# Kernel tuning notes

Hardware: AMD Instinct MI355X
Metric: run time of the kernel (lower is better)

## Reference

```python
import jax, jax.numpy as jnp
import numpy as np

D_MODEL = 1024
NUM_HEADS = 16
D_K = D_MODEL // NUM_HEADS  # 64
MAX_REL_POS = 16
B, SQ, SK = 1, 2048, 2048


def setup_inputs() -> dict:
    key = jax.random.key(0)
    ks = jax.random.split(key, 12)
    s = 0.02
    inp = {
        "query": jax.random.normal(ks[0], (B, SQ, D_MODEL), jnp.float32),
        "key": jax.random.normal(ks[1], (B, SK, D_MODEL), jnp.float32),
        "value": jax.random.normal(ks[2], (B, SK, D_MODEL), jnp.float32),
        "mask": jnp.ones((B, 1, SQ, SK), dtype=bool),
        # torch nn.Linear weights: y = x @ W.T + b
        "Wq": jax.random.normal(ks[3], (D_MODEL, D_MODEL), jnp.float32) * s,
        "bq": jnp.zeros((D_MODEL,), jnp.float32),
        "Wk": jax.random.normal(ks[4], (D_MODEL, D_MODEL), jnp.float32) * s,
        "bk": jnp.zeros((D_MODEL,), jnp.float32),
        "Wv": jax.random.normal(ks[5], (D_MODEL, D_MODEL), jnp.float32) * s,
        "bv": jnp.zeros((D_MODEL,), jnp.float32),
        "Wo": jax.random.normal(ks[6], (D_MODEL, D_MODEL), jnp.float32) * s,
        "bo": jnp.zeros((D_MODEL,), jnp.float32),
        # RelativePosition embedding table: [2*P+1, d_k]
        "rel_table": jax.random.normal(ks[7], (2 * MAX_REL_POS + 1, D_K), jnp.float32) * s,
    }
    return inp


def reference(query, key, value, mask, Wq, bq, Wk, bk, Wv, bv, Wo, bo, rel_table):
    b, sq, d = query.shape
    sk = key.shape[1]
    H, dk = NUM_HEADS, D_K

    Q = (query @ Wq.T + bq).reshape(b, sq, H, dk).transpose(0, 2, 1, 3)  # [B,H,Sq,dk]
    K = (key @ Wk.T + bk).reshape(b, sk, H, dk).transpose(0, 2, 1, 3)    # [B,H,Sk,dk]
    V = (value @ Wv.T + bv).reshape(b, sk, H, dk).transpose(0, 2, 1, 3)  # [B,H,Sk,dk]

    scores = jnp.einsum("bhqd,bhkd->bhqk", Q, K)  # [B,H,Sq,Sk]

    # relative-position bias on keys: ref_pos[i,j] = clip(j-i, -P, P) + P
    pos = jnp.clip(jnp.arange(sk)[None, :] - jnp.arange(sq)[:, None],
                   -MAX_REL_POS, MAX_REL_POS) + MAX_REL_POS  # [Sq,Sk] int
    rel = rel_table[pos]  # [Sq,Sk,dk]
    scores = scores + jnp.einsum("bhqd,qkd->bhqk", Q, rel)

    scores = scores / jnp.sqrt(jnp.float32(dk))
    scores = jnp.where(mask, scores, jnp.float32(-1e12))
    attn = jax.nn.softmax(scores, axis=-1)

    x = jnp.einsum("bhqk,bhkd->bhqd", attn, V)  # [B,H,Sq,dk]
    x = x.transpose(0, 2, 1, 3).reshape(b, sq, d)
    return x @ Wo.T + bo
```

## Files before the change

### kernel.cpp

```cpp
#include <hip/hip_runtime.h>

#define S_LEN 2048
#define DM    1024
#define NH    16
#define DK    64
#define NP    33
#define QB    128
#define KB    64
#define NSPLIT 3

#define LOG2E 1.44269504088896340736f

typedef __attribute__((ext_vector_type(8))) __bf16 bf16x8;
typedef __attribute__((ext_vector_type(4))) float f32x4;
typedef __attribute__((ext_vector_type(16))) float f32x16;
typedef __attribute__((ext_vector_type(8))) unsigned short u16x8;

__device__ __forceinline__ unsigned short f2bf(float f) {
  unsigned int x = __float_as_uint(f);
  x += 0x7fffu + ((x >> 16) & 1u);
  return (unsigned short)(x >> 16);
}
__device__ __forceinline__ float bf2f(unsigned short u) {
  return __uint_as_float(((unsigned int)u) << 16);
}
__device__ __forceinline__ f32x4 mfma16(bf16x8 a, bf16x8 b, f32x4 c) {
  return __builtin_amdgcn_mfma_f32_16x16x32_bf16(a, b, c, 0, 0, 0);
}
__device__ __forceinline__ f32x16 mfma32(bf16x8 a, bf16x8 b, f32x16 c) {
  return __builtin_amdgcn_mfma_f32_32x32x16_bf16(a, b, c, 0, 0, 0);
}
__device__ __forceinline__ unsigned cvtpk(float lo, float hi) {
  unsigned r;
  asm("v_cvt_pk_bf16_f32 %0, %1, %2" : "=v"(r) : "v"(lo), "v"(hi));
  return r;
}
__device__ __forceinline__ void halfswap(unsigned &a, unsigned &b) {
  asm volatile("v_permlane32_swap_b32 %0, %1" : "+v"(a), "+v"(b));
}
__device__ __forceinline__ void gload16(const void* g, void* l) {
  __builtin_amdgcn_global_load_lds(
      (const __attribute__((address_space(1))) unsigned int*)g,
      (__attribute__((address_space(3))) unsigned int*)l, 16, 0, 0);
}
#define WAITCNT(n) asm volatile("s_waitcnt vmcnt(" #n ")" ::: "memory")
#define LGKM0 asm volatile("s_waitcnt lgkmcnt(0)" ::: "memory")
__device__ __forceinline__ void bar() { __builtin_amdgcn_s_barrier(); }
__device__ __forceinline__ u16x8 pk8(float4 a, float4 b) {
  union { unsigned u[4]; u16x8 v; } f;
  f.u[0] = cvtpk(a.x, a.y); f.u[1] = cvtpk(a.z, a.w);
  f.u[2] = cvtpk(b.x, b.y); f.u[3] = cvtpk(b.z, b.w);
  return f.v;
}

__global__ __launch_bounds__(256) void cvt_w_kernel(
    const float* wq, const float* wk, const float* wv, const float* wo,
    unsigned short* wqo, unsigned short* wko, unsigned short* wvo, unsigned short* woo)
{
#pragma unroll
  for (int j = 0; j < 4; j++) {
    int idx = blockIdx.x * 1024 + j * 256 + threadIdx.x;
    int sel = idx >> 17, off = idx & 131071;
    const float* s = sel == 0 ? wq : (sel == 1 ? wk : (sel == 2 ? wv : wo));
    unsigned short* d = sel == 0 ? wqo : (sel == 1 ? wko : (sel == 2 ? wvo : woo));
    const float* p = s + (size_t)off * 8;
    u16x8 o;
#pragma unroll
    for (int e = 0; e < 8; e++) o[e] = f2bf(p[e]);
    *(u16x8*)(d + (size_t)off * 8) = o;
  }
}

__global__ __launch_bounds__(256, 3) void gemm_qkv_kernel(
    const float* X0, const float* X1, const float* X2,
    const unsigned short* W0, const unsigned short* W1, const unsigned short* W2,
    const float* b0, const float* b1, const float* b2,
    unsigned short* O0, unsigned short* O1, unsigned short* VTout)
{
  __shared__ unsigned short As[2][64 * 64];
  __shared__ unsigned short Bs[2][128 * 64];
  int bid = blockIdx.x;
  int xcd = bid & 7, local = bid >> 3;
  int z = local >> 5, r = local & 31;
  int bn = (r & 7) * 128;
  int bm = (xcd * 4 + (r >> 3)) * 64;

  const float* A          = z == 0 ? X0 : (z == 1 ? X1 : X2);
  const unsigned short* W = z == 0 ? W0 : (z == 1 ? W1 : W2);
  const float* bias       = z == 0 ? b0 : (z == 1 ? b1 : b2);
  float scale             = z == 0 ? 0.125f * LOG2E : 1.f;

  int tid = threadIdx.x, lane = tid & 63, w = tid >> 6;
  int r15 = lane & 15, g = lane >> 4;
  int wm = (w & 1) * 32, wn = (w >> 1) * 64;
  f32x4 acc[2][4];
#pragma unroll
  for (int mi = 0; mi < 2; mi++)
#pragma unroll
    for (int ni = 0; ni < 4; ni++)
#pragma unroll
      for (int i = 0; i < 4; i++) acc[mi][ni][i] = 0.f;

  int ra0 = tid >> 3, sa0 = ((tid & 7) ^ (ra0 & 7)) * 8;
  int ra1 = ra0 + 32, sa1 = (((tid + 256) & 7) ^ (ra1 & 7)) * 8;
  const float* aF0 = &A[(size_t)(bm + ra0) * DM + sa0];
  const float* aF1 = &A[(size_t)(bm + ra1) * DM + sa1];
  const unsigned short* bSrc[4];
#pragma unroll
  for (int j = 0; j < 4; j++) {
    int cb = j * 256 + tid;
    int rb = cb >> 3, sb = ((cb & 7) ^ (rb & 7)) * 8;
    bSrc[j] = &W[(size_t)(bn + rb) * DM + sb];
  }

  float4 a00, a01, a10, a11;
  auto LOAD_A = [&](int k0) {
    a00 = *(const float4*)(aF0 + k0);     a01 = *(const float4*)(aF0 + k0 + 4);
    a10 = *(const float4*)(aF1 + k0);     a11 = *(const float4*)(aF1 + k0 + 4);
  };
  auto STAGE_B = [&](int b, int k0) {
#pragma unroll
    for (int j = 0; j < 4; j++) gload16(bSrc[j] + k0, &Bs[b][(j * 256 + tid) * 8]);
  };
  auto WRITE_A = [&](int b) {
    *(u16x8*)&As[b][tid * 8]         = pk8(a00, a01);
    *(u16x8*)&As[b][(tid + 256) * 8] = pk8(a10, a11);
  };

  const int NS = DM / 64;
  STAGE_B(0, 0);
  LOAD_A(0);
  WAITCNT(0);
  WRITE_A(0);
  LGKM0;
  bar();

  for (int s = 0; s < NS; s++) {
    int cur = s & 1;
    int k0 = s * 64;
    if (s + 1 < NS) { STAGE_B(cur ^ 1, k0 + 64); LOAD_A(k0 + 64); }
    bf16x8 af[2][2], bfr[4][2];
#pragma unroll
    for (int mi = 0; mi < 2; mi++) {
      int row = wm + mi * 16 + r15;
#pragma unroll
      for (int hf = 0; hf < 2; hf++)
        af[mi][hf] = *(const bf16x8*)&As[cur][row * 64 + (((hf * 4 + g) ^ (row & 7)) << 3)];
    }
#pragma unroll
    for (int ni = 0; ni < 4; ni++) {
      int row = wn + ni * 16 + r15;
#pragma unroll
      for (int hf = 0; hf < 2; hf++)
        bfr[ni][hf] = *(const bf16x8*)&Bs[cur][row * 64 + (((hf * 4 + g) ^ (row & 7)) << 3)];
    }
    __builtin_amdgcn_s_setprio(1);
#pragma unroll
    for (int hf = 0; hf < 2; hf++)
#pragma unroll
      for (int mi = 0; mi < 2; mi++)
#pragma unroll
        for (int ni = 0; ni < 4; ni++)
          acc[mi][ni] = mfma16(af[mi][hf], bfr[ni][hf], acc[mi][ni]);
    __builtin_amdgcn_s_setprio(0);
    if (s + 1 < NS) {
      WAITCNT(0);
      WRITE_A(cur ^ 1);
    }
    LGKM0;
    bar();
  }

  if (z < 2) {
    unsigned short* O = z == 0 ? O0 : O1;
#pragma unroll
    for (int mi = 0; mi < 2; mi++)
#pragma unroll
      for (int ni = 0; ni < 4; ni++) {
        int col = bn + wn + ni * 16 + r15;
        float bv = bias[col];
#pragma unroll
        for (int i = 0; i < 4; i++) {
          int row = bm + wm + mi * 16 + g * 4 + i;
          O[(size_t)row * DM + col] = f2bf((acc[mi][ni][i] + bv) * scale);
        }
      }
  } else {
    unsigned short* Tl = (unsigned short*)Bs;
    const int TP = 72;
#pragma unroll
    for (int mi = 0; mi < 2; mi++)
#pragma unroll
      for (int ni = 0; ni < 4; ni++) {
        int colL = wn + ni * 16 + r15;
        float bv = bias[bn + colL];
#pragma unroll
        for (int i = 0; i < 4; i++) {
          int rowL = wm + mi * 16 + g * 4 + i;
          Tl[colL * TP + rowL] = f2bf(acc[mi][ni][i] + bv);
        }
      }
    __syncthreads();
#pragma unroll
    for (int i = 0; i < 4; i++) {
      int c = i * 256 + tid;
      int colL = c >> 3, k8 = (c & 7) * 8;
      u16x8 vv = *(const u16x8*)&Tl[colL * TP + k8];
      *(u16x8*)&VTout[(size_t)(bn + colL) * S_LEN + bm + k8] = vv;
    }
  }
}

template<int MR, int NR, int F32OUT>
__device__ __forceinline__ void gemm_body(
    const unsigned short* __restrict__ A, const unsigned short* __restrict__ W,
    const float* __restrict__ bias, unsigned short* __restrict__ outb,
    float* __restrict__ outf, int N, int K, int bm, int bn, float scale)
{
  __shared__ unsigned short As[2][MR * 32 * 64];
  __shared__ unsigned short Bs[2][NR * 32 * 64];
  int tid = threadIdx.x, lane = tid & 63, w = tid >> 6;
  int r15 = lane & 15, g = lane >> 4;
  int wm = (w & 1) * (MR * 16), wn = (w >> 1) * (NR * 16);
  f32x4 acc[MR][NR];
#pragma unroll
  for (int mi = 0; mi < MR; mi++)
#pragma unroll
    for (int ni = 0; ni < NR; ni++)
#pragma unroll
      for (int i = 0; i < 4; i++) acc[mi][ni][i] = 0.f;

  int lc = w * 64 + lane;
  int lrow = lc >> 3;
  int lk = ((lc & 7) ^ (lrow & 7)) * 8;
  const unsigned short* aS = &A[(size_t)(bm + lrow) * K + lk];
  const unsigned short* bS = &W[(size_t)(bn + lrow) * K + lk];
  int wOff = w * 512;

  auto STAGE = [&](int b, int k0) {
#pragma unroll
    for (int j = 0; j < MR; j++)
      gload16(aS + (size_t)(32 * j) * K + k0, &As[b][j * 2048 + wOff]);
#pragma unroll
    for (int j = 0; j < NR; j++)
      gload16(bS + (size_t)(32 * j) * K + k0, &Bs[b][j * 2048 + wOff]);
  };

  const int NS = K / 64;
  STAGE(0, 0);
  WAITCNT(0);
  bar();
  for (int s = 0; s < NS; s++) {
    int cur = s & 1;
    int k0 = s * 64;
    if (s + 1 < NS) STAGE(cur ^ 1, k0 + 64);
    bf16x8 af[MR][2], bfr[NR][2];
#pragma unroll
    for (int mi = 0; mi < MR; mi++) {
      int row = wm + mi * 16 + r15;
#pragma unroll
      for (int hf = 0; hf < 2; hf++)
        af[mi][hf] = *(const bf16x8*)&As[cur][row * 64 + (((hf * 4 + g) ^ (row & 7)) << 3)];
    }
#pragma unroll
    for (int ni = 0; ni < NR; ni++) {
      int row = wn + ni * 16 + r15;
#pragma unroll
      for (int hf = 0; hf < 2; hf++)
        bfr[ni][hf] = *(const bf16x8*)&Bs[cur][row * 64 + (((hf * 4 + g) ^ (row & 7)) << 3)];
    }
    __builtin_amdgcn_s_setprio(1);
#pragma unroll
    for (int hf = 0; hf < 2; hf++)
#pragma unroll
      for (int mi = 0; mi < MR; mi++)
#pragma unroll
        for (int ni = 0; ni < NR; ni++)
          acc[mi][ni] = mfma16(af[mi][hf], bfr[ni][hf], acc[mi][ni]);
    __builtin_amdgcn_s_setprio(0);
    WAITCNT(0);
    bar();
  }
#pragma unroll
  for (int mi = 0; mi < MR; mi++)
#pragma unroll
    for (int ni = 0; ni < NR; ni++) {
      int col = bn + wn + ni * 16 + r15;
      float bv = bias[col];
#pragma unroll
      for (int i = 0; i < 4; i++) {
        int row = bm + wm + mi * 16 + g * 4 + i;
        float v = (acc[mi][ni][i] + bv) * scale;
        if (F32OUT) outf[(size_t)row * N + col] = v;
        else        outb[(size_t)row * N + col] = f2bf(v);
      }
    }
}

__global__ __launch_bounds__(256, 2) void gemm_out_kernel(
    const unsigned short* A, const unsigned short* W, const float* bias, float* out)
{
  int bid = blockIdx.x;
  int xcd = bid & 7, local = bid >> 3;
  int bn = (local & 15) * 64;
  int bm = (xcd * 4 + (local >> 4)) * 64;
  gemm_body<2, 2, 1>(A, W, bias, nullptr, out, DM, DM, bm, bn, 1.f);
}

__global__ __launch_bounds__(256) void qrel_kernel(
    const unsigned short* __restrict__ Qb, const float* __restrict__ rel,
    unsigned short* __restrict__ QRbT)
{
  __shared__ float rels[NP * DK];
  int h = blockIdx.y;
  int tid = threadIdx.x;
  int q = blockIdx.x * 256 + tid;
  for (int i = tid; i < NP * DK; i += 256) rels[i] = rel[i];
  __syncthreads();
  float qv[DK];
  const unsigned short* qp = &Qb[(size_t)q * DM + h * DK];
#pragma unroll
  for (int j = 0; j < 8; j++) {
    u16x8 v = *(const u16x8*)&qp[j * 8];
#pragma unroll
    for (int e = 0; e < 8; e++) qv[j * 8 + e] = bf2f(v[e]);
  }
  int qt = q >> 7, qloc = q & 127;
  unsigned short* outp = &QRbT[((size_t)(h * 16 + qt) * NP) * QB + qloc];
  for (int p = 0; p < NP; p++) {
    float s = 0.f;
#pragma unroll
    for (int d = 0; d < DK; d++) s += qv[d] * rels[p * DK + d];
    outp[p * QB] = f2bf(s);
  }
}

__global__ __launch_bounds__(256, 3) void attn_kernel(
    const unsigned short* __restrict__ Qb, const unsigned short* __restrict__ Kb,
    const unsigned short* __restrict__ VT, const unsigned short* __restrict__ QRbT,
    unsigned short* __restrict__ Opart, float* __restrict__ ml)
{
  __shared__ unsigned short Ks[2][KB * DK];
  __shared__ unsigned short Vs[2][DK * KB];
  __shared__ unsigned short QRs[NP * QB];

  int bid = blockIdx.x;
  int wid = (bid & 7) * 96 + (bid >> 3);
  int h  = wid / 48;
  int rem = wid - h * 48;
  int split = rem >> 4;
  int qt = rem & 15;
  int q0 = qt * QB;
  int tstart = split * 11;
  int ts = split == 2 ? 10 : 11;

  int tid = threadIdx.x;
  int l = tid & 63, w = tid >> 6;
  int lq = l & 31, hi = l >> 5;

  int c0 = tid, c1 = tid + 256;
  int r0 = c0 >> 3, s0 = ((c0 & 7) ^ (r0 & 7)) * 8;
  int r1 = c1 >> 3, s1 = ((c1 & 7) ^ (r1 & 7)) * 8;
  int db0 = w * 512, db1 = 2048 + w * 512;
  const unsigned short* Ksrc0 = &Kb[(size_t)r0 * DM + h * DK + s0];
  const unsigned short* Ksrc1 = &Kb[(size_t)r1 * DM + h * DK + s1];
  const unsigned short* Vsrc0 = &VT[((size_t)h * DK + r0) * S_LEN + s0];
  const unsigned short* Vsrc1 = &VT[((size_t)h * DK + r1) * S_LEN + s1];

  auto STAGE = [&](int buf, int kb) {
    gload16(Ksrc0 + (size_t)kb * DM, &Ks[buf][db0]);
    gload16(Ksrc1 + (size_t)kb * DM, &Ks[buf][db1]);
    gload16(Vsrc0 + kb, &Vs[buf][db0]);
    gload16(Vsrc1 + kb, &Vs[buf][db1]);
  };

  int kb0 = tstart * KB;
  STAGE(0, kb0);

  {
    const u16x8* qsrc = (const u16x8*)&QRbT[(size_t)(h * 16 + qt) * NP * QB];
    u16x8* qdst = (u16x8*)QRs;
    for (int i = tid; i < NP * QB / 8; i += 256) qdst[i] = qsrc[i];
  }

  int qglob = q0 + w * 32 + lq;
  int qcol = w * 32 + lq;
  const unsigned short* qp = &Qb[(size_t)qglob * DM + h * DK + hi * 8];
  bf16x8 qfs[4];
#pragma unroll
  for (int s = 0; s < 4; s++) qfs[s] = *(const bf16x8*)&qp[s * 16];

  float m_i = -1e30f, l_i = 0.f;
  f32x16 o0, o1;
#pragma unroll
  for (int r = 0; r < 16; r++) { o0[r] = 0.f; o1[r] = 0.f; }

  asm volatile("s_waitcnt vmcnt(0) lgkmcnt(0)" ::: "memory");
  bar();

  for (int t = 0; t < ts; t++) {
    int buf = t & 1;
    int kbase = (tstart + t) * KB;
    if (t + 1 < ts) STAGE(buf ^ 1, kbase + KB);

    f32x16 sT0, sT1;
#pragma unroll
    for (int r = 0; r < 16; r++) { sT0[r] = 0.f; sT1[r] = 0.f; }
    __builtin_amdgcn_s_setprio(1);
#pragma unroll
    for (int s = 0; s < 4; s++) {
      int ch = s * 2 + hi;
      bf16x8 k0 = *(const bf16x8*)&Ks[buf][(lq) * DK + ((ch ^ (lq & 7)) << 3)];
      bf16x8 k1 = *(const bf16x8*)&Ks[buf][(32 + lq) * DK + ((ch ^ (lq & 7)) << 3)];
      sT0 = mfma32(k0, qfs[s], sT0);
      sT1 = mfma32(k1, qfs[s], sT1);
    }
    __builtin_amdgcn_s_setprio(0);

    bool hiC = (kbase - (q0 + QB - 1)) >= 16;
    bool loC = ((kbase + KB - 1) - q0) <= -16;
    float c_u = 0.f;
    if (hiC || loC) {
      c_u = bf2f(QRs[(hiC ? 32 : 0) * QB + qcol]);
    } else {
#pragma unroll
      for (int r = 0; r < 16; r++) {
        int km = (r & 3) + ((r >> 2) << 3) + (hi << 2);
        int d0 = kbase + km - qglob;
        int i0 = d0 < -16 ? 0 : (d0 > 16 ? 32 : d0 + 16);
        sT0[r] += bf2f(QRs[i0 * QB + qcol]);
        int d1 = d0 + 32;
        int i1 = d1 < -16 ? 0 : (d1 > 16 ? 32 : d1 + 16);
        sT1[r] += bf2f(QRs[i1 * QB + qcol]);
      }
    }

    float a0 = fmaxf(sT0[0], sT1[0]), a1 = fmaxf(sT0[1], sT1[1]);
    float a2 = fmaxf(sT0[2], sT1[2]), a3 = fmaxf(sT0[3], sT1[3]);
#pragma unroll
    for (int r = 4; r < 16; r += 4) {
      a0 = fmaxf(a0, fmaxf(sT0[r], sT1[r]));
      a1 = fmaxf(a1, fmaxf(sT0[r + 1], sT1[r + 1]));
      a2 = fmaxf(a2, fmaxf(sT0[r + 2], sT1[r + 2]));
      a3 = fmaxf(a3, fmaxf(sT0[r + 3], sT1[r + 3]));
    }
    float tm = fmaxf(fmaxf(a0, a1), fmaxf(a2, a3));
    tm = fmaxf(tm, __shfl_xor(tm, 32));
    float eff = tm + c_u;
    if (!__all(eff <= m_i + 11.5f)) {
      float mn = fmaxf(m_i, eff);
      float sc = __builtin_amdgcn_exp2f(m_i - mn);
      m_i = mn; l_i *= sc;
#pragma unroll
      for (int r = 0; r < 16; r++) { o0[r] *= sc; o1[r] *= sc; }
    }
    float mc = m_i - c_u;
    float p[32];
    float ls0 = 0.f, ls1 = 0.f, ls2 = 0.f, ls3 = 0.f;
#pragma unroll
    for (int r = 0; r < 16; r += 4) {
      p[r]     = __builtin_amdgcn_exp2f(sT0[r] - mc);     ls0 += p[r];
      p[r + 1] = __builtin_amdgcn_exp2f(sT0[r + 1] - mc); ls1 += p[r + 1];
      p[r + 2] = __builtin_amdgcn_exp2f(sT0[r + 2] - mc); ls2 += p[r + 2];
      p[r + 3] = __builtin_amdgcn_exp2f(sT0[r + 3] - mc); ls3 += p[r + 3];
    }
#pragma unroll
    for (int r = 0; r < 16; r += 4) {
      p[16 + r]     = __builtin_amdgcn_exp2f(sT1[r] - mc);     ls0 += p[16 + r];
      p[16 + r + 1] = __builtin_amdgcn_exp2f(sT1[r + 1] - mc); ls1 += p[16 + r + 1];
      p[16 + r + 2] = __builtin_amdgcn_exp2f(sT1[r + 2] - mc); ls2 += p[16 + r + 2];
      p[16 + r + 3] = __builtin_amdgcn_exp2f(sT1[r + 3] - mc); ls3 += p[16 + r + 3];
    }
    float ls = (ls0 + ls1) + (ls2 + ls3);
    ls += __shfl_xor(ls, 32);
    l_i += ls;

    bf16x8 pf[4];
#pragma unroll
    for (int kg = 0; kg < 2; kg++) {
      const float* pp = &p[kg * 16];
#pragma unroll
      for (int s2 = 0; s2 < 2; s2++) {
        unsigned b1 = cvtpk(pp[s2 * 8 + 0], pp[s2 * 8 + 1]);
        unsigned b2 = cvtpk(pp[s2 * 8 + 4], pp[s2 * 8 + 5]);
        unsigned b3 = cvtpk(pp[s2 * 8 + 2], pp[s2 * 8 + 3]);
        unsigned b4 = cvtpk(pp[s2 * 8 + 6], pp[s2 * 8 + 7]);
        halfswap(b1, b2); halfswap(b3, b4);
        union { unsigned u[4]; bf16x8 v; } f;
        f.u[0] = b1; f.u[1] = b3; f.u[2] = b2; f.u[3] = b4;
        pf[kg * 2 + s2] = f.v;
      }
    }

    __builtin_amdgcn_s_setprio(1);
#pragma unroll
    for (int s = 0; s < 4; s++) {
      int ch = s * 2 + hi;
      bf16x8 v0 = *(const bf16x8*)&Vs[buf][(lq) * KB + ((ch ^ (lq & 7)) << 3)];
      bf16x8 v1 = *(const bf16x8*)&Vs[buf][(32 + lq) * KB + ((ch ^ (lq & 7)) << 3)];
      o0 = mfma32(v0, pf[s], o0);
      o1 = mfma32(v1, pf[s], o1);
    }
    __builtin_amdgcn_s_setprio(0);

    WAITCNT(0);
    bar();
  }

  float inv = 1.f / l_i;
  unsigned* Ot32 = (unsigned*)Ks;
  int qloc = w * 32 + lq;
  int swz = (qloc & 7) << 3;
#pragma unroll
  for (int r = 0; r < 16; r += 2) {
    int d0 = (r & 3) + ((r >> 2) << 3) + (hi << 2);
    Ot32[qloc * 32 + (((d0) ^ swz) >> 1)]      = cvtpk(o0[r] * inv, o0[r + 1] * inv);
    Ot32[qloc * 32 + (((d0 + 32) ^ swz) >> 1)] = cvtpk(o1[r] * inv, o1[r + 1] * inv);
  }
  __syncthreads();
  unsigned short* Ot = (unsigned short*)Ks;
  size_t pb = ((size_t)(h * 16 + qt) * NSPLIT + split) * QB;
#pragma unroll
  for (int i = 0; i < 4; i++) {
    int c = i * 256 + tid;
    int q = c >> 3, ch = c & 7;
    *(u16x8*)&Opart[(pb + q) * DK + ch * 8] =
        *(const u16x8*)&Ot[q * 64 + ((ch ^ (q & 7)) << 3)];
  }
  if (hi == 0) {
    float2 v; v.x = m_i; v.y = l_i;
    *(float2*)&ml[(pb + qloc) * 2] = v;
  }
}

__global__ __launch_bounds__(256) void merge_kernel(
    const unsigned short* __restrict__ Opart, const float* __restrict__ ml,
    unsigned short* __restrict__ Xb)
{
  __shared__ float wsc[NSPLIT][QB];
  int qt = blockIdx.x, h = blockIdx.y;
  int tid = threadIdx.x;
  size_t pb = (size_t)(h * 16 + qt) * NSPLIT;
  if (tid < QB) {
    float m[NSPLIT], li[NSPLIT];
#pragma unroll
    for (int s = 0; s < NSPLIT; s++) {
      float2 v = *(const float2*)&ml[((pb + s) * QB + tid) * 2];
      m[s] = v.x; li[s] = v.y;
    }
    float mx = fmaxf(fmaxf(m[0], m[1]), m[2]);
    float t[NSPLIT], sum = 0.f;
#pragma unroll
    for (int s = 0; s < NSPLIT; s++) { t[s] = exp2f(m[s] - mx) * li[s]; sum += t[s]; }
    float inv = 1.f / sum;
#pragma unroll
    for (int s = 0; s < NSPLIT; s++) wsc[s][tid] = t[s] * inv;
  }
  __syncthreads();
  int q0 = qt * QB;
#pragma unroll
  for (int i = 0; i < 4; i++) {
    int c = i * 256 + tid;
    int q = c >> 3, d8 = (c & 7) * 8;
    float acc[8];
#pragma unroll
    for (int j = 0; j < 8; j++) acc[j] = 0.f;
#pragma unroll
    for (int s = 0; s < NSPLIT; s++) {
      u16x8 v = *(const u16x8*)&Opart[((pb + s) * QB + q) * DK + d8];
      float ws = wsc[s][q];
#pragma unroll
      for (int j = 0; j < 8; j++) acc[j] += ws * bf2f(v[j]);
    }
    u16x8 o;
#pragma unroll
    for (int j = 0; j < 8; j++) o[j] = f2bf(acc[j]);
    *(u16x8*)&Xb[(size_t)(q0 + q) * DM + h * DK + d8] = o;
  }
}

extern "C" void kernel_launch(void* const* d_in, const int* in_sizes, int n_in,
                              void* d_out, int out_size, void* d_ws, size_t ws_size,
                              hipStream_t stream) {
  const float* query = (const float*)d_in[0];
  const float* key_  = (const float*)d_in[1];
  const float* value = (const float*)d_in[2];
  const float* Wq = (const float*)d_in[4];
  const float* bq = (const float*)d_in[5];
  const float* Wk = (const float*)d_in[6];
  const float* bk = (const float*)d_in[7];
  const float* Wv = (const float*)d_in[8];
  const float* bv = (const float*)d_in[9];
  const float* Wo = (const float*)d_in[10];
  const float* bo = (const float*)d_in[11];
  const float* rel = (const float*)d_in[12];

  char* ws = (char*)d_ws;
  unsigned short* Opart = (unsigned short*)(ws + 0);
  float* mlbuf = (float*)(ws + 12582912);
  unsigned short* Wqb = (unsigned short*)(ws + 13369344);
  unsigned short* Wkb = (unsigned short*)(ws + 15466496);
  unsigned short* Wvb = (unsigned short*)(ws + 17563648);
  unsigned short* Wob = (unsigned short*)(ws + 19660800);
  unsigned short* Qb  = (unsigned short*)(ws + 21757952);
  unsigned short* Kb  = (unsigned short*)(ws + 25952256);
  unsigned short* VT  = (unsigned short*)(ws + 30146560);
  unsigned short* Xb  = (unsigned short*)(ws + 34340864);
  unsigned short* QRb = (unsigned short*)(ws + 38535168);

  cvt_w_kernel<<<dim3(512), dim3(256), 0, stream>>>(
      Wq, Wk, Wv, Wo, Wqb, Wkb, Wvb, Wob);

  gemm_qkv_kernel<<<dim3(768), dim3(256), 0, stream>>>(
      query, key_, value, Wqb, Wkb, Wvb, bq, bk, bv, Qb, Kb, VT);

  qrel_kernel<<<dim3(8, 16), dim3(256), 0, stream>>>(Qb, rel, QRb);

  attn_kernel<<<dim3(768), dim3(256), 0, stream>>>(Qb, Kb, VT, QRb, Opart, mlbuf);
  merge_kernel<<<dim3(16, 16), dim3(256), 0, stream>>>(Opart, mlbuf, Xb);

  gemm_out_kernel<<<dim3(512), dim3(256), 0, stream>>>(Xb, Wob, bo, (float*)d_out);
}
```

Before: 93.02 us.

## Split attention key range four ways and shrink LDS for higher occupancy

Raises the flash-decoding style key split from three to four, so 1024 attention blocks run with eight key tiles each instead of uneven 11/10 splits, and raises launch bounds to four blocks per CU. The relative-position table in LDS is cut from 33 to 32 rows, with the last bucket held in a register, so LDS per block drops enough to fit the higher occupancy. The aim is better load balance across the 256 CUs and more latency hiding. In exchange it adds a fourth partial output and softmax state to write and merge, a larger workspace, and register pressure under the tighter launch bound.

```diff
diff --git a/kernel.cpp b/kernel.cpp
--- a/kernel.cpp
+++ b/kernel.cpp
@@ -7,7 +7,8 @@
 #define NP    33
 #define QB    128
 #define KB    64
-#define NSPLIT 3
+#define NSPLIT 4
+#define TS    (S_LEN / KB / NSPLIT)
 
 #define LOG2E 1.44269504088896340736f
 
@@ -335,24 +336,23 @@
   }
 }
 
-__global__ __launch_bounds__(256, 3) void attn_kernel(
+__global__ __launch_bounds__(256, 4) void attn_kernel(
     const unsigned short* __restrict__ Qb, const unsigned short* __restrict__ Kb,
     const unsigned short* __restrict__ VT, const unsigned short* __restrict__ QRbT,
     unsigned short* __restrict__ Opart, float* __restrict__ ml)
 {
   __shared__ unsigned short Ks[2][KB * DK];
   __shared__ unsigned short Vs[2][DK * KB];
-  __shared__ unsigned short QRs[NP * QB];
+  __shared__ unsigned short QRs[32 * QB];
 
   int bid = blockIdx.x;
-  int wid = (bid & 7) * 96 + (bid >> 3);
-  int h  = wid / 48;
-  int rem = wid - h * 48;
+  int wid = (bid & 7) * 128 + (bid >> 3);
+  int h  = wid >> 6;
+  int rem = wid & 63;
   int split = rem >> 4;
   int qt = rem & 15;
   int q0 = qt * QB;
-  int tstart = split * 11;
-  int ts = split == 2 ? 10 : 11;
+  int tstart = split * TS;
 
   int tid = threadIdx.x;
   int l = tid & 63, w = tid >> 6;
@@ -377,14 +377,17 @@
   int kb0 = tstart * KB;
   STAGE(0, kb0);
 
+  const unsigned short* qrbase = &QRbT[(size_t)(h * 16 + qt) * NP * QB];
   {
-    const u16x8* qsrc = (const u16x8*)&QRbT[(size_t)(h * 16 + qt) * NP * QB];
+    const u16x8* qsrc = (const u16x8*)qrbase;
     u16x8* qdst = (u16x8*)QRs;
-    for (int i = tid; i < NP * QB / 8; i += 256) qdst[i] = qsrc[i];
+    for (int i = tid; i < 32 * QB / 8; i += 256) qdst[i] = qsrc[i];
   }
 
   int qglob = q0 + w * 32 + lq;
   int qcol = w * 32 + lq;
+  float qr32 = bf2f(qrbase[32 * QB + qcol]);
+
   const unsigned short* qp = &Qb[(size_t)qglob * DM + h * DK + hi * 8];
   bf16x8 qfs[4];
 #pragma unroll
@@ -398,10 +401,10 @@
   asm volatile("s_waitcnt vmcnt(0) lgkmcnt(0)" ::: "memory");
   bar();
 
-  for (int t = 0; t < ts; t++) {
+  for (int t = 0; t < TS; t++) {
     int buf = t & 1;
     int kbase = (tstart + t) * KB;
-    if (t + 1 < ts) STAGE(buf ^ 1, kbase + KB);
+    if (t + 1 < TS) STAGE(buf ^ 1, kbase + KB);
 
     f32x16 sT0, sT1;
 #pragma unroll
@@ -421,17 +424,19 @@
     bool loC = ((kbase + KB - 1) - q0) <= -16;
     float c_u = 0.f;
     if (hiC || loC) {
-      c_u = bf2f(QRs[(hiC ? 32 : 0) * QB + qcol]);
+      c_u = hiC ? qr32 : bf2f(QRs[qcol]);
     } else {
 #pragma unroll
       for (int r = 0; r < 16; r++) {
         int km = (r & 3) + ((r >> 2) << 3) + (hi << 2);
         int d0 = kbase + km - qglob;
         int i0 = d0 < -16 ? 0 : (d0 > 16 ? 32 : d0 + 16);
-        sT0[r] += bf2f(QRs[i0 * QB + qcol]);
+        float bl0 = bf2f(QRs[(i0 > 31 ? 31 : i0) * QB + qcol]);
+        sT0[r] += (i0 > 31) ? qr32 : bl0;
         int d1 = d0 + 32;
         int i1 = d1 < -16 ? 0 : (d1 > 16 ? 32 : d1 + 16);
-        sT1[r] += bf2f(QRs[i1 * QB + qcol]);
+        float bl1 = bf2f(QRs[(i1 > 31 ? 31 : i1) * QB + qcol]);
+        sT1[r] += (i1 > 31) ? qr32 : bl1;
       }
     }
 
@@ -548,7 +553,7 @@
       float2 v = *(const float2*)&ml[((pb + s) * QB + tid) * 2];
       m[s] = v.x; li[s] = v.y;
     }
-    float mx = fmaxf(fmaxf(m[0], m[1]), m[2]);
+    float mx = fmaxf(fmaxf(m[0], m[1]), fmaxf(m[2], m[3]));
     float t[NSPLIT], sum = 0.f;
 #pragma unroll
     for (int s = 0; s < NSPLIT; s++) { t[s] = exp2f(m[s] - mx) * li[s]; sum += t[s]; }
@@ -597,16 +602,16 @@
 
   char* ws = (char*)d_ws;
   unsigned short* Opart = (unsigned short*)(ws + 0);
-  float* mlbuf = (float*)(ws + 12582912);
-  unsigned short* Wqb = (unsigned short*)(ws + 13369344);
-  unsigned short* Wkb = (unsigned short*)(ws + 15466496);
-  unsigned short* Wvb = (unsigned short*)(ws + 17563648);
-  unsigned short* Wob = (unsigned short*)(ws + 19660800);
-  unsigned short* Qb  = (unsigned short*)(ws + 21757952);
-  unsigned short* Kb  = (unsigned short*)(ws + 25952256);
-  unsigned short* VT  = (unsigned short*)(ws + 30146560);
-  unsigned short* Xb  = (unsigned short*)(ws + 34340864);
-  unsigned short* QRb = (unsigned short*)(ws + 38535168);
+  float* mlbuf = (float*)(ws + 16777216);
+  unsigned short* Wqb = (unsigned short*)(ws + 17825792);
+  unsigned short* Wkb = (unsigned short*)(ws + 19922944);
+  unsigned short* Wvb = (unsigned short*)(ws + 22020096);
+  unsigned short* Wob = (unsigned short*)(ws + 24117248);
+  unsigned short* Qb  = (unsigned short*)(ws + 26214400);
+  unsigned short* Kb  = (unsigned short*)(ws + 30408704);
+  unsigned short* VT  = (unsigned short*)(ws + 34603008);
+  unsigned short* Xb  = (unsigned short*)(ws + 38797312);
+  unsigned short* QRb = (unsigned short*)(ws + 42991616);
 
   cvt_w_kernel<<<dim3(512), dim3(256), 0, stream>>>(
       Wq, Wk, Wv, Wo, Wqb, Wkb, Wvb, Wob);
@@ -616,7 +621,7 @@
 
   qrel_kernel<<<dim3(8, 16), dim3(256), 0, stream>>>(Qb, rel, QRb);
 
-  attn_kernel<<<dim3(768), dim3(256), 0, stream>>>(Qb, Kb, VT, QRb, Opart, mlbuf);
+  attn_kernel<<<dim3(1024), dim3(256), 0, stream>>>(Qb, Kb, VT, QRb, Opart, mlbuf);
   merge_kernel<<<dim3(16, 16), dim3(256), 0, stream>>>(Opart, mlbuf, Xb);
 
   gemm_out_kernel<<<dim3(512), dim3(256), 0, stream>>>(Xb, Wob, bo, (float*)d_out);
```

After: 104.5 us. 12.3% more time.
